# Kernel tuning notes

Measured on AMD Instinct MI355X. Metric: run time of the kernel, lower is better.

Reference implementation:

```python
import jax, jax.numpy as jnp
import numpy as np

GROUP_SIZES = [16, 16, 16, 16]
K = 2
TEMPERATURE = 1.0
NEG = float(np.finfo(np.float32).min)  # torch.finfo(dtype).min


def setup_inputs() -> dict:
    key = jax.random.key(0)
    k1, k2, k3 = jax.random.split(key, 3)
    B, S, D, E, G = 8, 4096, 1024, 64, len(GROUP_SIZES)
    x = jax.random.normal(k1, (B, S, D), dtype=jnp.float32)
    W_group = jax.random.normal(k2, (G, D), dtype=jnp.float32) * 0.02
    W_expert = jax.random.normal(k3, (E, D), dtype=jnp.float32) * 0.02
    return {"x": x, "W_group": W_group, "W_expert": W_expert}


def reference(x, W_group, W_expert):
    E = W_expert.shape[0]
    # group id of each expert (contiguous ranges) -- static
    expert_group = jnp.asarray(np.repeat(np.arange(len(GROUP_SIZES)), GROUP_SIZES))  # [E]

    # gate logits (no bias), temperature scaling
    expert_logits = jnp.einsum('bsd,ed->bse', x, W_expert) * (1.0 / TEMPERATURE)  # [B,S,E]
    group_logits = jnp.einsum('bsd,gd->bsg', x, W_group)                          # [B,S,G]
    group_probs = jax.nn.softmax(group_logits, axis=-1)
    g_idx = jnp.argmax(group_probs, axis=-1)                                      # [B,S]

    # mask experts outside the selected group's contiguous range
    mask = expert_group[None, None, :] != g_idx[..., None]                        # [B,S,E] bool
    mdt = mask.astype(expert_logits.dtype)
    masked_logits = mdt * NEG + (1.0 - mdt) * expert_logits

    probs_full = jax.nn.softmax(masked_logits, axis=-1)                           # [B,S,E]
    topk_vals, idx = jax.lax.top_k(masked_logits, K)                              # [B,S,K]
    scores = jax.nn.softmax(topk_vals, axis=-1)

    # aux stats (no_grad in original)
    importance = jax.lax.stop_gradient(jnp.mean(probs_full, axis=(0, 1)))         # [E]
    counts = jnp.zeros((E,), probs_full.dtype).at[idx.reshape(-1)].add(1.0)       # [E]
    load = counts / jnp.maximum(jnp.sum(counts), 1.0)
    return (idx, scores, probs_full, importance, load)
```

## Files before the change

### kernel.cpp

```cpp
#include <hip/hip_runtime.h>
#include <math.h>

#define TOKENS   32768
#define DDIM     1024
#define BK       32
#define NTILES   32
#define MT       64
#define NBLOCKS  (TOKENS/MT)

#define OFF_SCORES 65536
#define OFF_PROBS  131072
#define OFF_IMP    2228224
#define OFF_LOAD   2228288

#define XB0 0
#define WB0 2048
#define XB1 4640
#define WB1 6688
#define SCRA 0
#define SCRB 4672
#define ELOG 9344
#define CNTO 14016
#define SMEM_WORDS 14080

__global__ __launch_bounds__(256, 2)
void router_kernel(const float* __restrict__ x,
                   const float* __restrict__ Wg,
                   const float* __restrict__ We,
                   float* __restrict__ out,
                   float* __restrict__ ws) {
  __shared__ __attribute__((aligned(16))) float smem[SMEM_WORDS];
  const int tid  = threadIdx.x;
  const int lane = tid & 63;
  const int wv   = tid >> 6;
  const int tn   = lane & 7;
  const int tm   = lane >> 3;
  const int tok0 = blockIdx.x * MT;

  if (tid < 64) ((int*)(smem + CNTO))[tid] = 0;
  if (tid < 144) { smem[WB0 + 68*36 + tid] = 0.f; smem[WB1 + 68*36 + tid] = 0.f; }

  float acc[8][9];
  #pragma unroll
  for (int i = 0; i < 8; ++i)
    #pragma unroll
    for (int j = 0; j < 9; ++j) acc[i][j] = 0.f;

  auto do_load = [&](int kb, float4& xg0, float4& xg1, float4& wg0, float4& wg1, float4& wg2) {
    { int i2 = tid;       int kq = i2 & 7, t = i2 >> 3;
      xg0 = *(const float4*)(x + (size_t)(tok0 + t)*DDIM + kb + 4*kq); }
    { int i2 = tid + 256; int kq = i2 & 7, t = i2 >> 3;
      xg1 = *(const float4*)(x + (size_t)(tok0 + t)*DDIM + kb + 4*kq); }
    { int i2 = tid;       int kq = i2 & 7, r = i2 >> 3;
      wg0 = *(const float4*)(We + (size_t)r*DDIM + kb + 4*kq); }
    { int i2 = tid + 256; int kq = i2 & 7, r = i2 >> 3;
      wg1 = *(const float4*)(We + (size_t)r*DDIM + kb + 4*kq); }
    if (tid < 32) { int kq = tid & 7; int r = (tid + 512) >> 3;
      wg2 = *(const float4*)(Wg + (size_t)(r - 64)*DDIM + kb + 4*kq); }
  };
  auto do_store = [&](int xoff, int woff, float4 xg0, float4 xg1, float4 wg0, float4 wg1, float4 wg2) {
    { int i2 = tid;       int kq = i2 & 7, t = i2 >> 3;
      *(float4*)(smem + xoff + t*32 + 4*(kq ^ (t >> 3))) = xg0; }
    { int i2 = tid + 256; int kq = i2 & 7, t = i2 >> 3;
      *(float4*)(smem + xoff + t*32 + 4*(kq ^ (t >> 3))) = xg1; }
    { int i2 = tid;       int kq = i2 & 7, r = i2 >> 3;
      *(float4*)(smem + woff + r*36 + 4*kq) = wg0; }
    { int i2 = tid + 256; int kq = i2 & 7, r = i2 >> 3;
      *(float4*)(smem + woff + r*36 + 4*kq) = wg1; }
    if (tid < 32) { int kq = tid & 7; int r = (tid + 512) >> 3;
      *(float4*)(smem + woff + r*36 + 4*kq) = wg2; }
  };

  {
    float4 a = {0,0,0,0}, b = a, c = a, d = a, e = a;
    do_load(0, a, b, c, d, e);
    do_store(XB0, WB0, a, b, c, d, e);
  }
  __syncthreads();

  const int xoffs[2] = {XB0, XB1}, woffs[2] = {WB0, WB1};

  for (int tile = 0; tile < NTILES; ++tile) {
    const int p = tile & 1;
    float4 xg0 = {0,0,0,0}, xg1 = xg0, wg0 = xg0, wg1 = xg0, wg2 = xg0;
    const bool pf = (tile + 1 < NTILES);
    if (pf) do_load((tile + 1) * BK, xg0, xg1, wg0, wg1, wg2);

    const float* xb = smem + xoffs[p];
    const float* wb = smem + woffs[p];
    #pragma unroll
    for (int qi = 0; qi < 2; ++qi) {
      const int kq = (wv << 1) | qi;
      const float* xptr = xb + tm*256 + 4*(kq ^ tm);
      const float* wptr = wb + tn*324 + 4*kq;
      float4 xr[8], wr[9];
      #pragma unroll
      for (int i = 0; i < 8; ++i) xr[i] = *(const float4*)(xptr + i*32);
      #pragma unroll
      for (int j = 0; j < 9; ++j) wr[j] = *(const float4*)(wptr + j*36);
      #pragma unroll
      for (int i = 0; i < 8; ++i)
        #pragma unroll
        for (int j = 0; j < 9; ++j) {
          acc[i][j] = fmaf(xr[i].x, wr[j].x, acc[i][j]);
          acc[i][j] = fmaf(xr[i].y, wr[j].y, acc[i][j]);
          acc[i][j] = fmaf(xr[i].z, wr[j].z, acc[i][j]);
          acc[i][j] = fmaf(xr[i].w, wr[j].w, acc[i][j]);
        }
    }
    if (pf) do_store(xoffs[p ^ 1], woffs[p ^ 1], xg0, xg1, wg0, wg1, wg2);
    __syncthreads();
  }

  {
    float* A  = smem + SCRA;
    float* Bv = smem + SCRB;
    const int rb = lane * 73;
    if (wv == 1) {
      #pragma unroll
      for (int i = 0; i < 8; ++i)
        #pragma unroll
        for (int j = 0; j < 9; ++j) A[rb + i*9 + j] = acc[i][j];
    }
    if (wv == 3) {
      #pragma unroll
      for (int i = 0; i < 8; ++i)
        #pragma unroll
        for (int j = 0; j < 9; ++j) Bv[rb + i*9 + j] = acc[i][j];
    }
    __syncthreads();
    if (wv == 0) {
      #pragma unroll
      for (int i = 0; i < 8; ++i)
        #pragma unroll
        for (int j = 0; j < 9; ++j) acc[i][j] += A[rb + i*9 + j];
    }
    if (wv == 2) {
      #pragma unroll
      for (int i = 0; i < 8; ++i)
        #pragma unroll
        for (int j = 0; j < 9; ++j) acc[i][j] += Bv[rb + i*9 + j];
    }
    __syncthreads();
    if (wv == 2) {
      #pragma unroll
      for (int i = 0; i < 8; ++i)
        #pragma unroll
        for (int j = 0; j < 9; ++j) A[rb + i*9 + j] = acc[i][j];
    }
    __syncthreads();
    if (wv == 0) {
      float* el = smem + ELOG;
      #pragma unroll
      for (int i = 0; i < 8; ++i)
        #pragma unroll
        for (int j = 0; j < 9; ++j) {
          const float v = acc[i][j] + A[rb + i*9 + j];
          el[(tm*8 + i)*73 + (tn*9 + j)] = v;
        }
    }
    __syncthreads();
  }

  float* el  = smem + ELOG;
  int*   cnt = (int*)(smem + CNTO);
  if (tid < 64) {
    const int t = tid;
    float* row = el + t*73;
    const float g0 = row[64], g1 = row[65], g2 = row[66], g3 = row[67];
    int g = 0; float gb = g0;
    if (g1 > gb) { g = 1; gb = g1; }
    if (g2 > gb) { g = 2; gb = g2; }
    if (g3 > gb) { g = 3; gb = g3; }
    const int base = g << 4;
    float l[16];
    #pragma unroll
    for (int e = 0; e < 16; ++e) l[e] = row[base + e];
    int i1 = 0; float v1 = l[0];
    #pragma unroll
    for (int e = 1; e < 16; ++e) if (l[e] > v1) { i1 = e; v1 = l[e]; }
    int i2 = -1; float v2 = 0.f;
    #pragma unroll
    for (int e = 0; e < 16; ++e) {
      if (e == i1) continue;
      if (i2 < 0 || l[e] > v2) { i2 = e; v2 = l[e]; }
    }
    float pr[16]; float s = 0.f;
    #pragma unroll
    for (int e = 0; e < 16; ++e) { pr[e] = expf(l[e] - v1); s += pr[e]; }
    const float inv = 1.f / s;
    #pragma unroll
    for (int c = 0; c < 64; ++c) row[c] = 0.f;
    #pragma unroll
    for (int e = 0; e < 16; ++e) row[base + e] = pr[e] * inv;
    const size_t T = (size_t)tok0 + t;
    out[2*T]     = (float)(base + i1);
    out[2*T + 1] = (float)(base + i2);
    const float e2 = expf(v2 - v1);
    const float si = 1.f / (1.f + e2);
    out[OFF_SCORES + 2*T]     = si;
    out[OFF_SCORES + 2*T + 1] = e2 * si;
    atomicAdd(&cnt[base + i1], 1);
    atomicAdd(&cnt[base + i2], 1);
  }
  __syncthreads();

  for (int i = tid; i < MT*64; i += 256) {
    const int t = i >> 6, c = i & 63;
    out[OFF_PROBS + (((size_t)(tok0 + t)) << 6) + c] = el[t*73 + c];
  }
  if (tid < 64) {
    const int e = tid;
    float s = 0.f;
    for (int t = 0; t < MT; ++t) s += el[t*73 + e];
    atomicAdd(&ws[e], s);
    atomicAdd(&ws[64 + e], (float)cnt[e]);
  }
}

__global__ void finalize_kernel(const float* __restrict__ ws, float* __restrict__ out) {
  const int e = threadIdx.x;
  if (e < 64) {
    out[OFF_IMP  + e] = ws[e]      * (1.0f / 32768.0f);
    out[OFF_LOAD + e] = ws[64 + e] * (1.0f / 65536.0f);
  }
}

extern "C" void kernel_launch(void* const* d_in, const int* in_sizes, int n_in,
                              void* d_out, int out_size, void* d_ws, size_t ws_size,
                              hipStream_t stream) {
  (void)in_sizes; (void)n_in; (void)out_size; (void)ws_size;
  const float* x  = (const float*)d_in[0];
  const float* Wg = (const float*)d_in[1];
  const float* We = (const float*)d_in[2];
  float* out = (float*)d_out;
  float* ws  = (float*)d_ws;
  hipMemsetAsync(d_ws, 0, 128 * sizeof(float), stream);
  hipLaunchKernelGGL(router_kernel, dim3(NBLOCKS), dim3(256), 0, stream, x, Wg, We, out, ws);
  hipLaunchKernelGGL(finalize_kernel, dim3(1), dim3(64), 0, stream, ws, out);
}
```

Before: 253.2 us.

## Replace FP32 FMA GEMM with split-bf16x3 MFMA using prepacked weight fragments

Replaces the shared-memory-tiled FP32 FMA GEMM with bf16 MFMA instructions. Each fp32 operand is split into three bf16 pieces and multiplied with eight MFMAs per tile to approximate fp32 accuracy. A new prep kernel packs the weights into MFMA fragment layout in a global buffer. x is read straight from global memory with no LDS staging, and the K dimension is split across wave pairs with an LDS reduction. This trades extra MFMA work and the split arithmetic for matrix-core throughput, and adds a kernel launch plus a small precision risk in argmax and top-k ties.

```diff
diff --git a/kernel.cpp b/kernel.cpp
--- a/kernel.cpp
+++ b/kernel.cpp
@@ -3,170 +3,163 @@
 
 #define TOKENS   32768
 #define DDIM     1024
-#define BK       32
-#define NTILES   32
-#define MT       64
-#define NBLOCKS  (TOKENS/MT)
+#define NBLOCKS  512
 
 #define OFF_SCORES 65536
 #define OFF_PROBS  131072
 #define OFF_IMP    2228224
 #define OFF_LOAD   2228288
 
-#define XB0 0
-#define WB0 2048
-#define XB1 4640
-#define WB1 6688
-#define SCRA 0
-#define SCRB 4672
-#define ELOG 9344
-#define CNTO 14016
-#define SMEM_WORDS 14080
+typedef __attribute__((ext_vector_type(8))) short  short8;
+typedef __attribute__((ext_vector_type(4))) float  f32x4;
+typedef __attribute__((ext_vector_type(4))) int    intx4;
+
+__device__ __attribute__((aligned(16))) short wfrag[32 * 5 * 3 * 64 * 8];
+
+__device__ inline unsigned rne_hi(float x) {
+  unsigned u = __float_as_uint(x);
+  unsigned r = u + 0x7fffu + ((u >> 16) & 1u);
+  return r & 0xffff0000u;
+}
+
+__device__ inline void split3(const float* xv, short8& f1, short8& f2, short8& f3) {
+  int o1[4], o2[4], o3[4];
+  #pragma unroll
+  for (int p = 0; p < 4; ++p) {
+    float x0 = xv[2*p], x1 = xv[2*p+1];
+    unsigned h0 = rne_hi(x0), h1 = rne_hi(x1);
+    o1[p] = (int)((h0 >> 16) | (h1 & 0xffff0000u));
+    float r0 = x0 - __uint_as_float(h0);
+    float r1 = x1 - __uint_as_float(h1);
+    unsigned g0 = rne_hi(r0), g1 = rne_hi(r1);
+    o2[p] = (int)((g0 >> 16) | (g1 & 0xffff0000u));
+    float s0 = r0 - __uint_as_float(g0);
+    float s1 = r1 - __uint_as_float(g1);
+    unsigned w0 = rne_hi(s0), w1 = rne_hi(s1);
+    o3[p] = (int)((w0 >> 16) | (w1 & 0xffff0000u));
+  }
+  intx4 t1 = {o1[0], o1[1], o1[2], o1[3]};
+  intx4 t2 = {o2[0], o2[1], o2[2], o2[3]};
+  intx4 t3 = {o3[0], o3[1], o3[2], o3[3]};
+  f1 = __builtin_bit_cast(short8, t1);
+  f2 = __builtin_bit_cast(short8, t2);
+  f3 = __builtin_bit_cast(short8, t3);
+}
+
+__global__ void prep_kernel(const float* __restrict__ Wg, const float* __restrict__ We) {
+  const int nt   = blockIdx.x >> 5;
+  const int ks   = blockIdx.x & 31;
+  const int lane = threadIdx.x & 63;
+  const int row  = nt * 16 + (lane & 15);
+  const int k0   = ks * 32 + (lane >> 4) * 8;
+  float xv[8];
+  #pragma unroll
+  for (int j = 0; j < 8; ++j) {
+    float v = 0.f;
+    if (row < 64)      v = We[(size_t)row * DDIM + k0 + j];
+    else if (row < 68) v = Wg[(size_t)(row - 64) * DDIM + k0 + j];
+    xv[j] = v;
+  }
+  short8 f1, f2, f3;
+  split3(xv, f1, f2, f3);
+  short8* dst = (short8*)wfrag + (((size_t)ks * 5 + nt) * 3) * 64 + lane;
+  dst[0]   = f1;
+  dst[64]  = f2;
+  dst[128] = f3;
+}
 
 __global__ __launch_bounds__(256, 2)
 void router_kernel(const float* __restrict__ x,
-                   const float* __restrict__ Wg,
-                   const float* __restrict__ We,
                    float* __restrict__ out,
                    float* __restrict__ ws) {
-  __shared__ __attribute__((aligned(16))) float smem[SMEM_WORDS];
-  const int tid  = threadIdx.x;
-  const int lane = tid & 63;
-  const int wv   = tid >> 6;
-  const int tn   = lane & 7;
-  const int tm   = lane >> 3;
-  const int tok0 = blockIdx.x * MT;
-
-  if (tid < 64) ((int*)(smem + CNTO))[tid] = 0;
-  if (tid < 144) { smem[WB0 + 68*36 + tid] = 0.f; smem[WB1 + 68*36 + tid] = 0.f; }
-
-  float acc[8][9];
+  __shared__ float el[64 * 88];
+  __shared__ int   cnt[64];
+  const int tid    = threadIdx.x;
+  const int lane   = tid & 63;
+  const int wv     = tid >> 6;
+  const int tokgrp = wv >> 1;
+  const int khalf  = wv & 1;
+  const int quad   = lane >> 4;
+  const int m      = lane & 15;
+  const int tokblk = blockIdx.x * 64;
+  const int tok0   = tokblk + tokgrp * 32;
+
+  if (tid < 64) cnt[tid] = 0;
+
+  const float* ap0 = x + (size_t)(tok0 + m) * DDIM + khalf * 512 + quad * 8;
+  const float* ap1 = ap0 + (size_t)16 * DDIM;
+
+  f32x4 ahi[2][5], alo[2][5];
   #pragma unroll
-  for (int i = 0; i < 8; ++i)
-    #pragma unroll
-    for (int j = 0; j < 9; ++j) acc[i][j] = 0.f;
-
-  auto do_load = [&](int kb, float4& xg0, float4& xg1, float4& wg0, float4& wg1, float4& wg2) {
-    { int i2 = tid;       int kq = i2 & 7, t = i2 >> 3;
-      xg0 = *(const float4*)(x + (size_t)(tok0 + t)*DDIM + kb + 4*kq); }
-    { int i2 = tid + 256; int kq = i2 & 7, t = i2 >> 3;
-      xg1 = *(const float4*)(x + (size_t)(tok0 + t)*DDIM + kb + 4*kq); }
-    { int i2 = tid;       int kq = i2 & 7, r = i2 >> 3;
-      wg0 = *(const float4*)(We + (size_t)r*DDIM + kb + 4*kq); }
-    { int i2 = tid + 256; int kq = i2 & 7, r = i2 >> 3;
-      wg1 = *(const float4*)(We + (size_t)r*DDIM + kb + 4*kq); }
-    if (tid < 32) { int kq = tid & 7; int r = (tid + 512) >> 3;
-      wg2 = *(const float4*)(Wg + (size_t)(r - 64)*DDIM + kb + 4*kq); }
-  };
-  auto do_store = [&](int xoff, int woff, float4 xg0, float4 xg1, float4 wg0, float4 wg1, float4 wg2) {
-    { int i2 = tid;       int kq = i2 & 7, t = i2 >> 3;
-      *(float4*)(smem + xoff + t*32 + 4*(kq ^ (t >> 3))) = xg0; }
-    { int i2 = tid + 256; int kq = i2 & 7, t = i2 >> 3;
-      *(float4*)(smem + xoff + t*32 + 4*(kq ^ (t >> 3))) = xg1; }
-    { int i2 = tid;       int kq = i2 & 7, r = i2 >> 3;
-      *(float4*)(smem + woff + r*36 + 4*kq) = wg0; }
-    { int i2 = tid + 256; int kq = i2 & 7, r = i2 >> 3;
-      *(float4*)(smem + woff + r*36 + 4*kq) = wg1; }
-    if (tid < 32) { int kq = tid & 7; int r = (tid + 512) >> 3;
-      *(float4*)(smem + woff + r*36 + 4*kq) = wg2; }
-  };
-
-  {
-    float4 a = {0,0,0,0}, b = a, c = a, d = a, e = a;
-    do_load(0, a, b, c, d, e);
-    do_store(XB0, WB0, a, b, c, d, e);
+  for (int mt = 0; mt < 2; ++mt)
+    #pragma unroll
+    for (int nt = 0; nt < 5; ++nt) { ahi[mt][nt] = 0.f; alo[mt][nt] = 0.f; }
+
+  for (int ks = 0; ks < 16; ++ks) {
+    const float* p0 = ap0 + ks * 32;
+    const float* p1 = ap1 + ks * 32;
+    float4 a0 = *(const float4*)(p0), a1 = *(const float4*)(p0 + 4);
+    float4 a2 = *(const float4*)(p1), a3 = *(const float4*)(p1 + 4);
+
+    const short8* bp = (const short8*)wfrag + ((size_t)(khalf * 16 + ks) * 15) * 64 + lane;
+    short8 fb[5][3];
+    #pragma unroll
+    for (int nt = 0; nt < 5; ++nt) {
+      fb[nt][0] = bp[nt * 192];
+      fb[nt][1] = bp[nt * 192 + 64];
+      fb[nt][2] = bp[nt * 192 + 128];
+    }
+    short8 fa[2][3];
+    {
+      float av[8] = {a0.x, a0.y, a0.z, a0.w, a1.x, a1.y, a1.z, a1.w};
+      split3(av, fa[0][0], fa[0][1], fa[0][2]);
+      float bv[8] = {a2.x, a2.y, a2.z, a2.w, a3.x, a3.y, a3.z, a3.w};
+      split3(bv, fa[1][0], fa[1][1], fa[1][2]);
+    }
+    #pragma unroll
+    for (int nt = 0; nt < 5; ++nt)
+      #pragma unroll
+      for (int mt = 0; mt < 2; ++mt) {
+        ahi[mt][nt] = __builtin_amdgcn_mfma_f32_16x16x32_bf16(fa[mt][0], fb[nt][0], ahi[mt][nt], 0, 0, 0);
+        f32x4 c = alo[mt][nt];
+        c = __builtin_amdgcn_mfma_f32_16x16x32_bf16(fa[mt][0], fb[nt][1], c, 0, 0, 0);
+        c = __builtin_amdgcn_mfma_f32_16x16x32_bf16(fa[mt][1], fb[nt][0], c, 0, 0, 0);
+        c = __builtin_amdgcn_mfma_f32_16x16x32_bf16(fa[mt][1], fb[nt][1], c, 0, 0, 0);
+        c = __builtin_amdgcn_mfma_f32_16x16x32_bf16(fa[mt][0], fb[nt][2], c, 0, 0, 0);
+        c = __builtin_amdgcn_mfma_f32_16x16x32_bf16(fa[mt][2], fb[nt][0], c, 0, 0, 0);
+        c = __builtin_amdgcn_mfma_f32_16x16x32_bf16(fa[mt][1], fb[nt][2], c, 0, 0, 0);
+        c = __builtin_amdgcn_mfma_f32_16x16x32_bf16(fa[mt][2], fb[nt][1], c, 0, 0, 0);
+        alo[mt][nt] = c;
+      }
+  }
+
+  if (khalf == 1) {
+    #pragma unroll
+    for (int mt = 0; mt < 2; ++mt)
+      #pragma unroll
+      for (int nt = 0; nt < 5; ++nt)
+        #pragma unroll
+        for (int r = 0; r < 4; ++r)
+          el[(tokgrp * 32 + mt * 16 + quad * 4 + r) * 88 + nt * 16 + m] =
+              ahi[mt][nt][r] + alo[mt][nt][r];
   }
   __syncthreads();
-
-  const int xoffs[2] = {XB0, XB1}, woffs[2] = {WB0, WB1};
-
-  for (int tile = 0; tile < NTILES; ++tile) {
-    const int p = tile & 1;
-    float4 xg0 = {0,0,0,0}, xg1 = xg0, wg0 = xg0, wg1 = xg0, wg2 = xg0;
-    const bool pf = (tile + 1 < NTILES);
-    if (pf) do_load((tile + 1) * BK, xg0, xg1, wg0, wg1, wg2);
-
-    const float* xb = smem + xoffs[p];
-    const float* wb = smem + woffs[p];
-    #pragma unroll
-    for (int qi = 0; qi < 2; ++qi) {
-      const int kq = (wv << 1) | qi;
-      const float* xptr = xb + tm*256 + 4*(kq ^ tm);
-      const float* wptr = wb + tn*324 + 4*kq;
-      float4 xr[8], wr[9];
+  if (khalf == 0) {
+    #pragma unroll
+    for (int mt = 0; mt < 2; ++mt)
       #pragma unroll
-      for (int i = 0; i < 8; ++i) xr[i] = *(const float4*)(xptr + i*32);
-      #pragma unroll
-      for (int j = 0; j < 9; ++j) wr[j] = *(const float4*)(wptr + j*36);
-      #pragma unroll
-      for (int i = 0; i < 8; ++i)
+      for (int nt = 0; nt < 5; ++nt)
         #pragma unroll
-        for (int j = 0; j < 9; ++j) {
-          acc[i][j] = fmaf(xr[i].x, wr[j].x, acc[i][j]);
-          acc[i][j] = fmaf(xr[i].y, wr[j].y, acc[i][j]);
-          acc[i][j] = fmaf(xr[i].z, wr[j].z, acc[i][j]);
-          acc[i][j] = fmaf(xr[i].w, wr[j].w, acc[i][j]);
+        for (int r = 0; r < 4; ++r) {
+          const int idx = (tokgrp * 32 + mt * 16 + quad * 4 + r) * 88 + nt * 16 + m;
+          el[idx] += ahi[mt][nt][r] + alo[mt][nt][r];
         }
-    }
-    if (pf) do_store(xoffs[p ^ 1], woffs[p ^ 1], xg0, xg1, wg0, wg1, wg2);
-    __syncthreads();
-  }
-
-  {
-    float* A  = smem + SCRA;
-    float* Bv = smem + SCRB;
-    const int rb = lane * 73;
-    if (wv == 1) {
-      #pragma unroll
-      for (int i = 0; i < 8; ++i)
-        #pragma unroll
-        for (int j = 0; j < 9; ++j) A[rb + i*9 + j] = acc[i][j];
-    }
-    if (wv == 3) {
-      #pragma unroll
-      for (int i = 0; i < 8; ++i)
-        #pragma unroll
-        for (int j = 0; j < 9; ++j) Bv[rb + i*9 + j] = acc[i][j];
-    }
-    __syncthreads();
-    if (wv == 0) {
-      #pragma unroll
-      for (int i = 0; i < 8; ++i)
-        #pragma unroll
-        for (int j = 0; j < 9; ++j) acc[i][j] += A[rb + i*9 + j];
-    }
-    if (wv == 2) {
-      #pragma unroll
-      for (int i = 0; i < 8; ++i)
-        #pragma unroll
-        for (int j = 0; j < 9; ++j) acc[i][j] += Bv[rb + i*9 + j];
-    }
-    __syncthreads();
-    if (wv == 2) {
-      #pragma unroll
-      for (int i = 0; i < 8; ++i)
-        #pragma unroll
-        for (int j = 0; j < 9; ++j) A[rb + i*9 + j] = acc[i][j];
-    }
-    __syncthreads();
-    if (wv == 0) {
-      float* el = smem + ELOG;
-      #pragma unroll
-      for (int i = 0; i < 8; ++i)
-        #pragma unroll
-        for (int j = 0; j < 9; ++j) {
-          const float v = acc[i][j] + A[rb + i*9 + j];
-          el[(tm*8 + i)*73 + (tn*9 + j)] = v;
-        }
-    }
-    __syncthreads();
-  }
-
-  float* el  = smem + ELOG;
-  int*   cnt = (int*)(smem + CNTO);
+  }
+  __syncthreads();
+
   if (tid < 64) {
     const int t = tid;
-    float* row = el + t*73;
+    float* row = el + t * 88;
     const float g0 = row[64], g1 = row[65], g2 = row[66], g3 = row[67];
     int g = 0; float gb = g0;
     if (g1 > gb) { g = 1; gb = g1; }
@@ -193,7 +186,7 @@
     for (int c = 0; c < 64; ++c) row[c] = 0.f;
     #pragma unroll
     for (int e = 0; e < 16; ++e) row[base + e] = pr[e] * inv;
-    const size_t T = (size_t)tok0 + t;
+    const size_t T = (size_t)tokblk + t;
     out[2*T]     = (float)(base + i1);
     out[2*T + 1] = (float)(base + i2);
     const float e2 = expf(v2 - v1);
@@ -205,14 +198,14 @@
   }
   __syncthreads();
 
-  for (int i = tid; i < MT*64; i += 256) {
+  for (int i = tid; i < 64 * 64; i += 256) {
     const int t = i >> 6, c = i & 63;
-    out[OFF_PROBS + (((size_t)(tok0 + t)) << 6) + c] = el[t*73 + c];
+    out[OFF_PROBS + (((size_t)(tokblk + t)) << 6) + c] = el[t * 88 + c];
   }
   if (tid < 64) {
     const int e = tid;
     float s = 0.f;
-    for (int t = 0; t < MT; ++t) s += el[t*73 + e];
+    for (int t = 0; t < 64; ++t) s += el[t * 88 + e];
     atomicAdd(&ws[e], s);
     atomicAdd(&ws[64 + e], (float)cnt[e]);
   }
@@ -236,6 +229,7 @@
   float* out = (float*)d_out;
   float* ws  = (float*)d_ws;
   hipMemsetAsync(d_ws, 0, 128 * sizeof(float), stream);
-  hipLaunchKernelGGL(router_kernel, dim3(NBLOCKS), dim3(256), 0, stream, x, Wg, We, out, ws);
+  hipLaunchKernelGGL(prep_kernel, dim3(160), dim3(64), 0, stream, Wg, We);
+  hipLaunchKernelGGL(router_kernel, dim3(NBLOCKS), dim3(256), 0, stream, x, out, ws);
   hipLaunchKernelGGL(finalize_kernel, dim3(1), dim3(64), 0, stream, ws, out);
 }
```

Result: faster. 221.7 us (-12.4%).
